# Kernel tuning notes

Measured on AMD Instinct MI355X. Metric: run time of the kernel, lower is better.

## Reference

```python
import jax, jax.numpy as jnp
import numpy as np

_INV_SQRT2 = np.float32(0.7071067811865476)


def _dwt_last(u):
    """Single-level Haar DWT along the last axis (pywt 'haar' convention).
    cA[i] = (u[2i]+u[2i+1])/sqrt(2), cD[i] = (u[2i]-u[2i+1])/sqrt(2)."""
    e = u[..., 0::2]
    o = u[..., 1::2]
    return (e + o) * _INV_SQRT2, (e - o) * _INV_SQRT2


def _dwt2(x):
    """Single-level 2D Haar DWT over the last two axes, matching pywt.dwt2.
    Returns (cA, cH, cV, cD) = ('aa', 'da', 'ad', 'dd') where the first
    letter is the filter applied along axis -2 and the second along axis -1."""
    a1, d1 = _dwt_last(x)                      # filter along axis -1
    a1t, d1t = a1.swapaxes(-1, -2), d1.swapaxes(-1, -2)
    aa, da = _dwt_last(a1t)                    # filter along axis -2
    ad, dd = _dwt_last(d1t)
    return (aa.swapaxes(-1, -2), da.swapaxes(-1, -2),
            ad.swapaxes(-1, -2), dd.swapaxes(-1, -2))


def setup_inputs() -> dict:
    key = jax.random.key(0)
    B, C, H, W = 32, 3, 512, 512
    x = jax.random.normal(key, (B, C, H, W), dtype=jnp.float32)
    return {"x": x}


def reference(x):
    # pywt.wavedec2(x, 'haar', level=2) -> [cA2, (cH2,cV2,cD2), (cH1,cV1,cD1)]
    a1, h1, v1, d1 = _dwt2(x)    # level 1: [B,C,H/2,W/2]
    a2, h2, v2, d2 = _dwt2(a1)   # level 2: [B,C,H/4,W/4]
    return (a2, h2, v2, d2, h1, v1, d1)
```

## Files before the change

### kernel.cpp

```cpp
#include <hip/hip_runtime.h>


#define KINV 0.7071067811865476f

typedef float v2f __attribute__((ext_vector_type(2)));
typedef float v4f __attribute__((ext_vector_type(4)));

__global__ __launch_bounds__(256) void haar2_fused_kernel(
    const float* __restrict__ x, float* __restrict__ out, int nimg)
{
    const int tid = blockIdx.x * blockDim.x + threadIdx.x;
    const int total = nimg << 13;
    if (tid >= total) return;

    const int c2  = tid & 127;
    const int rp  = (tid >> 7) & 63;
    const int img = tid >> 13;

    const float* xin = x + (size_t)img * (512 * 512);
    const int row0 = rp * 8;
    const int col0 = c2 * 4;

    float p[8][4];
    #pragma unroll
    for (int k = 0; k < 8; ++k) {
        v4f v = *reinterpret_cast<const v4f*>(xin + (size_t)(row0 + k) * 512 + col0);
        p[k][0] = v.x; p[k][1] = v.y; p[k][2] = v.z; p[k][3] = v.w;
    }

    float aa[4][2], da[4][2], ad[4][2], dd[4][2];
    #pragma unroll
    for (int i = 0; i < 4; ++i) {
        #pragma unroll
        for (int j = 0; j < 2; ++j) {
            const float p00 = p[2*i    ][2*j], p01 = p[2*i    ][2*j+1];
            const float p10 = p[2*i + 1][2*j], p11 = p[2*i + 1][2*j+1];
            const float sA = (p00 + p01) * KINV;
            const float sB = (p10 + p11) * KINV;
            const float dA = (p00 - p01) * KINV;
            const float dB = (p10 - p11) * KINV;
            aa[i][j] = (sA + sB) * KINV;
            da[i][j] = (sA - sB) * KINV;
            ad[i][j] = (dA + dB) * KINV;
            dd[i][j] = (dA - dB) * KINV;
        }
    }

    const size_t n2 = (size_t)nimg * 128 * 128;
    const size_t n1 = (size_t)nimg * 256 * 256;
    float* a2o = out;
    float* h2o = out + n2;
    float* v2o = out + 2 * n2;
    float* d2o = out + 3 * n2;
    float* h1o = out + 4 * n2;
    float* v1o = h1o + n1;
    float* d1o = h1o + 2 * n1;

    const size_t img1 = (size_t)img * 256 * 256;
    #pragma unroll
    for (int i = 0; i < 4; ++i) {
        const size_t off = img1 + (size_t)(4 * rp + i) * 256 + 2 * c2;
        v2f h = {da[i][0], da[i][1]};
        v2f v = {ad[i][0], ad[i][1]};
        v2f d = {dd[i][0], dd[i][1]};
        __builtin_nontemporal_store(h, reinterpret_cast<v2f*>(h1o + off));
        __builtin_nontemporal_store(v, reinterpret_cast<v2f*>(v1o + off));
        __builtin_nontemporal_store(d, reinterpret_cast<v2f*>(d1o + off));
    }

    #pragma unroll
    for (int h = 0; h < 2; ++h) {
        const int i0 = 2 * h;
        const float s0 = (aa[i0][0]     + aa[i0][1])     * KINV;
        const float d0 = (aa[i0][0]     - aa[i0][1])     * KINV;
        const float s1 = (aa[i0 + 1][0] + aa[i0 + 1][1]) * KINV;
        const float d1 = (aa[i0 + 1][0] - aa[i0 + 1][1]) * KINV;
        const size_t off2 = (size_t)img * 128 * 128 + (size_t)(2 * rp + h) * 128 + c2;
        __builtin_nontemporal_store((s0 + s1) * KINV, a2o + off2);
        __builtin_nontemporal_store((s0 - s1) * KINV, h2o + off2);
        __builtin_nontemporal_store((d0 + d1) * KINV, v2o + off2);
        __builtin_nontemporal_store((d0 - d1) * KINV, d2o + off2);
    }
}

extern "C" void kernel_launch(void* const* d_in, const int* in_sizes, int n_in,
                              void* d_out, int out_size, void* d_ws, size_t ws_size,
                              hipStream_t stream) {
    const float* x = (const float*)d_in[0];
    float* out = (float*)d_out;
    const int nimg = in_sizes[0] / (512 * 512);
    const int total = nimg << 13;
    const int block = 256;
    const int grid = (total + block - 1) / block;
    haar2_fused_kernel<<<grid, block, 0, stream>>>(x, out, nimg);
}
```

Baseline: 176.6 us.

## Stage Haar outputs through LDS to emit 16-byte coalesced stores

Each block now handles a 16-row strip of one image and writes all level-1 and level-2 subband results into shared memory. After a barrier, threads read them back and write 128-bit nontemporal vector stores, replacing the earlier 8-byte and 4-byte scattered stores. The goal is better write coalescing and fewer store instructions. The cost is about 32 KB of LDS per block, a block-wide sync, and extra LDS traffic, which can limit occupancy.

New measurement: 175.2 us. No clear change (-0.8%).

```diff
diff --git a/kernel.cpp b/kernel.cpp
--- a/kernel.cpp
+++ b/kernel.cpp
@@ -3,23 +3,26 @@
 
 #define KINV 0.7071067811865476f
 
+typedef float v4f __attribute__((ext_vector_type(4)));
 typedef float v2f __attribute__((ext_vector_type(2)));
-typedef float v4f __attribute__((ext_vector_type(4)));
 
 __global__ __launch_bounds__(256) void haar2_fused_kernel(
     const float* __restrict__ x, float* __restrict__ out, int nimg)
 {
-    const int tid = blockIdx.x * blockDim.x + threadIdx.x;
-    const int total = nimg << 13;
-    if (tid >= total) return;
+    __shared__ float lds1[3][8][256];
+    __shared__ float lds2[4][4][128];
 
-    const int c2  = tid & 127;
-    const int rp  = (tid >> 7) & 63;
-    const int img = tid >> 13;
+    const int t   = threadIdx.x;
+    const int bid = blockIdx.x;
+    const int by  = bid & 31;
+    const int img = bid >> 5;
+
+    const int cx = t & 127;
+    const int ry = t >> 7;
 
     const float* xin = x + (size_t)img * (512 * 512);
-    const int row0 = rp * 8;
-    const int col0 = c2 * 4;
+    const int row0 = by * 16 + ry * 8;
+    const int col0 = cx * 4;
 
     float p[8][4];
     #pragma unroll
@@ -28,9 +31,10 @@
         p[k][0] = v.x; p[k][1] = v.y; p[k][2] = v.z; p[k][3] = v.w;
     }
 
-    float aa[4][2], da[4][2], ad[4][2], dd[4][2];
+    float aa[4][2];
     #pragma unroll
     for (int i = 0; i < 4; ++i) {
+        float da[2], ad[2], dd[2];
         #pragma unroll
         for (int j = 0; j < 2; ++j) {
             const float p00 = p[2*i    ][2*j], p01 = p[2*i    ][2*j+1];
@@ -40,32 +44,14 @@
             const float dA = (p00 - p01) * KINV;
             const float dB = (p10 - p11) * KINV;
             aa[i][j] = (sA + sB) * KINV;
-            da[i][j] = (sA - sB) * KINV;
-            ad[i][j] = (dA + dB) * KINV;
-            dd[i][j] = (dA - dB) * KINV;
+            da[j]    = (sA - sB) * KINV;
+            ad[j]    = (dA + dB) * KINV;
+            dd[j]    = (dA - dB) * KINV;
         }
-    }
-
-    const size_t n2 = (size_t)nimg * 128 * 128;
-    const size_t n1 = (size_t)nimg * 256 * 256;
-    float* a2o = out;
-    float* h2o = out + n2;
-    float* v2o = out + 2 * n2;
-    float* d2o = out + 3 * n2;
-    float* h1o = out + 4 * n2;
-    float* v1o = h1o + n1;
-    float* d1o = h1o + 2 * n1;
-
-    const size_t img1 = (size_t)img * 256 * 256;
-    #pragma unroll
-    for (int i = 0; i < 4; ++i) {
-        const size_t off = img1 + (size_t)(4 * rp + i) * 256 + 2 * c2;
-        v2f h = {da[i][0], da[i][1]};
-        v2f v = {ad[i][0], ad[i][1]};
-        v2f d = {dd[i][0], dd[i][1]};
-        __builtin_nontemporal_store(h, reinterpret_cast<v2f*>(h1o + off));
-        __builtin_nontemporal_store(v, reinterpret_cast<v2f*>(v1o + off));
-        __builtin_nontemporal_store(d, reinterpret_cast<v2f*>(d1o + off));
+        const int lr = 4 * ry + i;
+        *reinterpret_cast<v2f*>(&lds1[0][lr][2 * cx]) = (v2f){da[0], da[1]};
+        *reinterpret_cast<v2f*>(&lds1[1][lr][2 * cx]) = (v2f){ad[0], ad[1]};
+        *reinterpret_cast<v2f*>(&lds1[2][lr][2 * cx]) = (v2f){dd[0], dd[1]};
     }
 
     #pragma unroll
@@ -75,11 +61,45 @@
         const float d0 = (aa[i0][0]     - aa[i0][1])     * KINV;
         const float s1 = (aa[i0 + 1][0] + aa[i0 + 1][1]) * KINV;
         const float d1 = (aa[i0 + 1][0] - aa[i0 + 1][1]) * KINV;
-        const size_t off2 = (size_t)img * 128 * 128 + (size_t)(2 * rp + h) * 128 + c2;
-        __builtin_nontemporal_store((s0 + s1) * KINV, a2o + off2);
-        __builtin_nontemporal_store((s0 - s1) * KINV, h2o + off2);
-        __builtin_nontemporal_store((d0 + d1) * KINV, v2o + off2);
-        __builtin_nontemporal_store((d0 - d1) * KINV, d2o + off2);
+        const int lr = 2 * ry + h;
+        lds2[0][lr][cx] = (s0 + s1) * KINV;
+        lds2[1][lr][cx] = (s0 - s1) * KINV;
+        lds2[2][lr][cx] = (d0 + d1) * KINV;
+        lds2[3][lr][cx] = (d0 - d1) * KINV;
+    }
+
+    __syncthreads();
+
+    const size_t n2 = (size_t)nimg * 128 * 128;
+    const size_t n1 = (size_t)nimg * 256 * 256;
+    float* outs1[3] = { out + 4 * n2, out + 4 * n2 + n1, out + 4 * n2 + 2 * n1 };
+    float* outs2[4] = { out, out + n2, out + 2 * n2, out + 3 * n2 };
+
+    const size_t img1 = (size_t)img * 256 * 256;
+    #pragma unroll
+    for (int arr = 0; arr < 3; ++arr) {
+        #pragma unroll
+        for (int r = 0; r < 2; ++r) {
+            const int idx = r * 256 + t;
+            const int row = idx >> 6;
+            const int c4  = idx & 63;
+            v4f v = *reinterpret_cast<const v4f*>(&lds1[arr][row][4 * c4]);
+            float* dst = outs1[arr] + img1 + (size_t)(8 * by + row) * 256 + 4 * c4;
+            __builtin_nontemporal_store(v, reinterpret_cast<v4f*>(dst));
+        }
+    }
+
+    const size_t img2 = (size_t)img * 128 * 128;
+    #pragma unroll
+    for (int r = 0; r < 2; ++r) {
+        const int idx = r * 256 + t;
+        const int arr = idx >> 7;
+        const int rem = idx & 127;
+        const int row = rem >> 5;
+        const int c4  = rem & 31;
+        v4f v = *reinterpret_cast<const v4f*>(&lds2[arr][row][4 * c4]);
+        float* dst = outs2[arr] + img2 + (size_t)(4 * by + row) * 128 + 4 * c4;
+        __builtin_nontemporal_store(v, reinterpret_cast<v4f*>(dst));
     }
 }
 
@@ -89,8 +109,6 @@
     const float* x = (const float*)d_in[0];
     float* out = (float*)d_out;
     const int nimg = in_sizes[0] / (512 * 512);
-    const int total = nimg << 13;
-    const int block = 256;
-    const int grid = (total + block - 1) / block;
-    haar2_fused_kernel<<<grid, block, 0, stream>>>(x, out, nimg);
+    const int grid = nimg * 32;
+    haar2_fused_kernel<<<grid, 256, 0, stream>>>(x, out, nimg);
 }
```
